# Kernel tuning notes

Hardware: AMD Instinct MI355X
Metric: run time of the kernel (lower is better)

## Reference

```python
import jax, jax.numpy as jnp
import numpy as np

MUL = 16            # multiplicity of 0e and 1o irreps (in and out)
N_NODES = 10000
N_EDGES = 160000
EDGE_FDIM = 128
H_DIM = 128
WNUM = 4 * MUL * MUL  # 4 instructions x (16 u x 1 v x 16 w) = 1024 weights per edge


def setup_inputs() -> dict:
    key = jax.random.key(0)
    ks = jax.random.split(key, 6)
    x = jax.random.normal(ks[0], (N_NODES, 4 * MUL), dtype=jnp.float32)  # 16x0e + 16x1o -> dim 64
    edge_index = jax.random.randint(ks[1], (2, N_EDGES), 0, N_NODES, dtype=jnp.int32)
    edge_attr = jax.random.normal(ks[2], (N_EDGES, EDGE_FDIM), dtype=jnp.float32)
    edge_sh = jax.random.normal(ks[3], (N_EDGES, 4), dtype=jnp.float32)  # 1x0e + 1x1o
    fc_w1 = jax.random.normal(ks[4], (EDGE_FDIM, H_DIM), dtype=jnp.float32) / np.sqrt(EDGE_FDIM)
    fc_b1 = jnp.zeros((H_DIM,), jnp.float32)
    fc_w2 = jax.random.normal(ks[5], (H_DIM, WNUM), dtype=jnp.float32) / np.sqrt(H_DIM)
    fc_b2 = jnp.zeros((WNUM,), jnp.float32)
    return dict(x=x, edge_index=edge_index, edge_attr=edge_attr, edge_sh=edge_sh,
                fc_w1=fc_w1, fc_b1=fc_b1, fc_w2=fc_w2, fc_b2=fc_b2)


def _tensor_product(xe, edge_sh, w):
    """FullyConnectedTensorProduct('16x0e+16x1o', '1x0e+1x1o', '16x0e+16x1o'),
    shared_weights=False. Instructions (uvw, v=1):
      0e x 0e -> 0e ; 0e x 1o -> 1o ; 1o x 0e -> 1o ; 1o x 1o -> 0e (dot / sqrt(3)).
    Path alpha = 1/sqrt(fan_in) with fan_in = 2*MUL per output irrep (2 paths x 16x1)."""
    x0 = xe[:, :MUL]                          # [E, 16] scalars
    x1 = xe[:, MUL:].reshape(-1, MUL, 3)      # [E, 16, 3] vectors
    sh0 = edge_sh[:, 0:1]                     # [E, 1]
    sh1 = edge_sh[:, 1:4]                     # [E, 3]
    wp = w.reshape(-1, 4, MUL, MUL)           # [E, 4 paths, u, w]
    w00, w01, w10, w11 = wp[:, 0], wp[:, 1], wp[:, 2], wp[:, 3]
    alpha = 1.0 / np.sqrt(2.0 * MUL)
    dot = jnp.einsum('eum,em->eu', x1, sh1)   # 1o . 1o -> 0e
    out0 = alpha * (jnp.einsum('eu,euw->ew', x0 * sh0, w00)
                    + jnp.einsum('eu,euw->ew', dot, w11) / np.sqrt(3.0))  # [E, 16]
    out1 = alpha * (jnp.einsum('eu,euw,em->ewm', x0, w01, sh1)
                    + jnp.einsum('eum,euw->ewm', x1 * sh0[:, :, None], w10))  # [E, 16, 3]
    return jnp.concatenate([out0, out1.reshape(-1, 3 * MUL)], axis=-1)  # [E, 64]


def reference(x, edge_index, edge_attr, edge_sh, fc_w1, fc_b1, fc_w2, fc_b2):
    src, dst = edge_index[0], edge_index[1]
    # per-edge tensor-product weights from edge features (dropout p=0 -> identity)
    w = jax.nn.relu(edge_attr @ fc_w1 + fc_b1) @ fc_w2 + fc_b2       # [E, 1024]
    tp_out = _tensor_product(x[src], edge_sh, w)                      # gather + TP
    seg = jax.ops.segment_sum(tp_out, dst, num_segments=N_NODES)      # scatter-add
    cnt = jax.ops.segment_sum(jnp.ones((N_EDGES,), tp_out.dtype), dst, num_segments=N_NODES)
    out = seg / jnp.maximum(cnt, 1.0)[:, None]                        # mean aggregation
    # residual: out_dim == in_dim (64), so F.pad is a no-op
    return out + x
```

## Files before the change

kernel.cpp:

```cpp
#include <hip/hip_runtime.h>
#include <stdint.h>

#define E_TOTAL 160000
#define NODES   10000
#define FDIM    128
#define HDIM    128
#define WN      1024
#define CDIM    64
#define EPB     32
#define NTHR    256

typedef __bf16 bf16x8 __attribute__((ext_vector_type(8)));
typedef __bf16 bf16x4 __attribute__((ext_vector_type(4)));
typedef float  f32x4  __attribute__((ext_vector_type(4)));

#define MFMA16(a,b,c) __builtin_amdgcn_mfma_f32_16x16x32_bf16(a,b,c,0,0,0)

#define WS_W1B (512*1024)
#define WS_CNT (576*1024)

__device__ __forceinline__ f32x4 ntload4(const float* p) {
    return __builtin_nontemporal_load((const f32x4*)p);
}

__global__ void prep_kernel(const float* __restrict__ W1, const float* __restrict__ W2,
                            __bf16* __restrict__ W1B, __bf16* __restrict__ W2B,
                            float* __restrict__ out_acc, int* __restrict__ cnt) {
    const int b   = blockIdx.x;
    const int tid = threadIdx.x;
    if (b < 72) {
        const float* W = (b < 64) ? W2 : W1;
        __bf16* outB   = (b < 64) ? W2B : W1B;
        const int N    = (b < 64) ? WN : HDIM;
        const int tile = (b < 64) ? b : (b - 64);
        const int lane = tid & 63, ks = tid >> 6;
        const int n  = tile * 16 + (lane & 15);
        const int k0 = ks * 32 + (lane >> 4) * 8;
        bf16x8 hi;
        #pragma unroll
        for (int j = 0; j < 8; ++j) hi[j] = (__bf16)W[(size_t)(k0 + j) * N + n];
        *(bf16x8*)(outB + ((size_t)(tile * 4 + ks) * 64 + lane) * 8) = hi;
    } else {
        const int zt = (b - 72) * NTHR + tid;
        const float4 z4 = make_float4(0.f, 0.f, 0.f, 0.f);
        for (int i = zt; i < NODES * CDIM / 4; i += 8 * NTHR) ((float4*)out_acc)[i] = z4;
        for (int i = zt; i < NODES; i += 8 * NTHR) cnt[i] = 0;
    }
}

__global__ __launch_bounds__(NTHR, 4)
void fused_edge_kernel(const float* __restrict__ x,
                       const int*   __restrict__ edge_index,
                       const float* __restrict__ edge_attr,
                       const float* __restrict__ edge_sh,
                       const float* __restrict__ fc_b1,
                       const float* __restrict__ fc_b2,
                       const __bf16* __restrict__ W1B,
                       const __bf16* __restrict__ W2B,
                       float* __restrict__ out_acc,
                       int*   __restrict__ cnt)
{
    __shared__ float s_f[6][16][EPB];
    __shared__ __align__(16) char s_ab[16384];
    __shared__ float s_b2s[WN];
    __shared__ float s_sh1[3][36];
    __shared__ int   s_dst[EPB];

    __bf16* s_attr = (__bf16*)s_ab;
    __bf16* s_h    = (__bf16*)(s_ab + 8192);

    const int tid  = threadIdx.x;
    const int w    = tid >> 6;
    const int th   = w >> 1;
    const int kh   = w & 1;
    const int lane = tid & 63;
    const int quad = lane >> 4;
    const int li   = lane & 15;
    const int e0   = blockIdx.x * EPB;

    if (lane < 32) {
        const int e  = lane;
        const int up = w * 4;
        const int ge = e0 + e;
        const int src = edge_index[ge];
        const f32x4 sh4 = ntload4(edge_sh + (size_t)ge * 4);
        if (tid < EPB) {
            const int d = edge_index[E_TOTAL + ge];
            s_dst[e] = d;
            atomicAdd(&cnt[d], 1);
            s_sh1[0][e] = sh4.y; s_sh1[1][e] = sh4.z; s_sh1[2][e] = sh4.w;
        }
        const float* xp = x + (size_t)src * CDIM;
        const float4 x0v = *(const float4*)(xp + up);
        const float4 xa  = *(const float4*)(xp + 16 + up * 3);
        const float4 xb  = *(const float4*)(xp + 16 + up * 3 + 4);
        const float4 xc  = *(const float4*)(xp + 16 + up * 3 + 8);
        const float x1v[4][3] = {
            {xa.x, xa.y, xa.z}, {xa.w, xb.x, xb.y},
            {xb.z, xb.w, xc.x}, {xc.y, xc.z, xc.w}};
        const float x0a[4] = {x0v.x, x0v.y, x0v.z, x0v.w};
        const float alpha = 0.17677669529663689f;
        const float ai3   = alpha * 0.57735026918962576f;
        const float sh0 = sh4.x;
        #pragma unroll
        for (int j = 0; j < 4; ++j) {
            const int u = up + j;
            const float x0u = x0a[j];
            s_f[0][u][e] = alpha * sh0 * x0u;
            s_f[1][u][e] = alpha * x0u;
            s_f[2][u][e] = alpha * sh0 * x1v[j][0];
            s_f[3][u][e] = alpha * sh0 * x1v[j][1];
            s_f[4][u][e] = alpha * sh0 * x1v[j][2];
            s_f[5][u][e] = ai3 * (x1v[j][0]*sh4.y + x1v[j][1]*sh4.z + x1v[j][2]*sh4.w);
        }
    }
    #pragma unroll
    for (int t4 = 0; t4 < 4; ++t4) {
        const int t = tid + t4 * NTHR;
        const int e = t >> 5, i4 = t & 31;
        const f32x4 v = ntload4(edge_attr + (size_t)(e0 + e) * FDIM + i4 * 4);
        const int f = i4 >> 3, j0 = (i4 & 1) * 4, qc = (i4 >> 1) & 3;
        const int g = e >> 4, lc = e & 15;
        bf16x4 bv = {(__bf16)v[0], (__bf16)v[1], (__bf16)v[2], (__bf16)v[3]};
        *(bf16x4*)(s_attr + (((f * 2 + g) * 64 + qc * 16 + lc) * 8 + j0)) = bv;
    }
    *(f32x4*)&s_b2s[tid * 4] = *(const f32x4*)(fc_b2 + tid * 4);
    __syncthreads();

    {
        const int nt0 = w * 2;
        const float b1a = fc_b1[nt0 * 16 + li];
        const float b1b = fc_b1[(nt0 + 1) * 16 + li];
        bf16x8 A1[2][4];
        #pragma unroll
        for (int g = 0; g < 2; ++g)
            #pragma unroll
            for (int ks = 0; ks < 4; ++ks)
                A1[g][ks] = *(const bf16x8*)(s_attr + ((ks * 2 + g) * 64 + lane) * 8);
        #pragma unroll
        for (int nt2 = 0; nt2 < 2; ++nt2) {
            const int nt = nt0 + nt2;
            const float bias = nt2 ? b1b : b1a;
            bf16x8 Bf[4];
            #pragma unroll
            for (int ks = 0; ks < 4; ++ks)
                Bf[ks] = *(const bf16x8*)(W1B + ((size_t)(nt * 4 + ks) * 64 + lane) * 8);
            f32x4 acc[2];
            #pragma unroll
            for (int g = 0; g < 2; ++g) acc[g] = (f32x4){bias, bias, bias, bias};
            #pragma unroll
            for (int ks = 0; ks < 4; ++ks)
                #pragma unroll
                for (int g = 0; g < 2; ++g) acc[g] = MFMA16(A1[g][ks], Bf[ks], acc[g]);
            const int f  = nt >> 1;
            const int qc = (2 * (nt & 1) + (li >> 3)) & 3;
            const int j  = li & 7;
            #pragma unroll
            for (int g = 0; g < 2; ++g)
                #pragma unroll
                for (int r = 0; r < 4; ++r)
                    s_h[((f * 2 + g) * 64 + qc * 16 + (quad * 4 + r)) * 8 + j] =
                        (__bf16)fmaxf(acc[g][r], 0.f);
        }
    }
    __syncthreads();

    bf16x8 A2[2][2];
    #pragma unroll
    for (int g = 0; g < 2; ++g)
        #pragma unroll
        for (int k2 = 0; k2 < 2; ++k2)
            A2[g][k2] = *(const bf16x8*)(s_h + (((kh * 2 + k2) * 2 + g) * 64 + lane) * 8);

    f32x4 o0[2];
    f32x4 o1[2][3];
    #pragma unroll
    for (int g = 0; g < 2; ++g) {
        o0[g] = (f32x4){0.f, 0.f, 0.f, 0.f};
        #pragma unroll
        for (int m = 0; m < 3; ++m) o1[g][m] = (f32x4){0.f, 0.f, 0.f, 0.f};
    }
    const int tbase = th * 32;
    const __bf16* Wp = W2B + ((size_t)(tbase * 4 + kh * 2) * 64 + lane) * 8;
    bf16x8 P[2][2];
    #pragma unroll
    for (int s = 0; s < 2; ++s)
        #pragma unroll
        for (int k2 = 0; k2 < 2; ++k2)
            P[s][k2] = *(const bf16x8*)(Wp + (s * 4 + k2) * 512);

    #pragma unroll
    for (int half = 0; half < 2; ++half) {
        #pragma unroll
        for (int cc = 0; cc < 16; ++cc) {
            const int c = half * 16 + cc;
            const int u = cc;
            const bf16x8 b0 = P[c & 1][0];
            const bf16x8 b1 = P[c & 1][1];
            if (c + 2 < 32) {
                #pragma unroll
                for (int k2 = 0; k2 < 2; ++k2)
                    P[c & 1][k2] = *(const bf16x8*)(Wp + ((c + 2) * 4 + k2) * 512);
            }
            f32x4 acc[2];
            if (kh == 0) {
                const float b2v = s_b2s[(tbase + c) * 16 + li];
                acc[0] = (f32x4){b2v, b2v, b2v, b2v};
                acc[1] = acc[0];
            } else {
                acc[0] = (f32x4){0.f, 0.f, 0.f, 0.f};
                acc[1] = acc[0];
            }
            #pragma unroll
            for (int g = 0; g < 2; ++g) {
                acc[g] = MFMA16(A2[g][0], b0, acc[g]);
                acc[g] = MFMA16(A2[g][1], b1, acc[g]);
            }
            if (th == 0) {
                if (half == 0) {
                    #pragma unroll
                    for (int g = 0; g < 2; ++g)
                        o0[g] += *(const f32x4*)&s_f[0][u][g * 16 + quad * 4] * acc[g];
                } else {
                    #pragma unroll
                    for (int g = 0; g < 2; ++g)
                        o1[g][0] += *(const f32x4*)&s_f[1][u][g * 16 + quad * 4] * acc[g];
                }
            } else {
                if (half == 0) {
                    #pragma unroll
                    for (int g = 0; g < 2; ++g)
                        #pragma unroll
                        for (int m = 0; m < 3; ++m)
                            o1[g][m] += *(const f32x4*)&s_f[2 + m][u][g * 16 + quad * 4] * acc[g];
                } else {
                    #pragma unroll
                    for (int g = 0; g < 2; ++g)
                        o0[g] += *(const f32x4*)&s_f[5][u][g * 16 + quad * 4] * acc[g];
                }
            }
        }
    }
    if (th == 0) {
        #pragma unroll
        for (int g = 0; g < 2; ++g) {
            const f32x4 t1 = o1[g][0];
            o1[g][2] = t1 * *(const f32x4*)&s_sh1[2][g * 16 + quad * 4];
            o1[g][1] = t1 * *(const f32x4*)&s_sh1[1][g * 16 + quad * 4];
            o1[g][0] = t1 * *(const f32x4*)&s_sh1[0][g * 16 + quad * 4];
        }
    }

    __syncthreads();
    float* regA = (float*)s_ab;
    float* regB = (float*)(s_ab + 8192);
    float* regC = &s_f[0][0][0];
    float* dump = (kh == 1) ? ((th == 0) ? regA : regB) : ((th == 1) ? regC : nullptr);
    if (dump) {
        #pragma unroll
        for (int g = 0; g < 2; ++g)
            #pragma unroll
            for (int r = 0; r < 4; ++r) {
                float* row = dump + (g * 16 + quad * 4 + r) * 64;
                row[li] = o0[g][r];
                #pragma unroll
                for (int m = 0; m < 3; ++m) row[16 + li * 3 + m] = o1[g][m][r];
            }
    }
    __syncthreads();
    if (kh == 0 && th == 0) {
        #pragma unroll
        for (int g = 0; g < 2; ++g)
            #pragma unroll
            for (int r = 0; r < 4; ++r) {
                const int e = g * 16 + quad * 4 + r;
                const float* rA = regA + e * 64;
                const float* rB = regB + e * 64;
                const float* rC = regC + e * 64;
                float* op = out_acc + (size_t)s_dst[e] * CDIM;
                unsafeAtomicAdd(&op[li], o0[g][r] + rA[li] + rB[li] + rC[li]);
                #pragma unroll
                for (int m = 0; m < 3; ++m) {
                    const int s = 16 + li * 3 + m;
                    unsafeAtomicAdd(&op[s], o1[g][m][r] + rA[s] + rB[s] + rC[s]);
                }
            }
    }
}

__global__ void finalize_kernel(const float* __restrict__ x,
                                const int*   __restrict__ cnt,
                                float*       __restrict__ out)
{
    const int idx = blockIdx.x * blockDim.x + threadIdx.x;
    if (idx < NODES * CDIM) {
        const int n = idx >> 6;
        const float c = (float)(cnt[n] > 1 ? cnt[n] : 1);
        out[idx] = out[idx] / c + x[idx];
    }
}

extern "C" void kernel_launch(void* const* d_in, const int* in_sizes, int n_in,
                              void* d_out, int out_size, void* d_ws, size_t ws_size,
                              hipStream_t stream) {
    (void)in_sizes; (void)n_in; (void)out_size; (void)ws_size;
    const float* x          = (const float*)d_in[0];
    const int*   edge_index = (const int*)  d_in[1];
    const float* edge_attr  = (const float*)d_in[2];
    const float* edge_sh    = (const float*)d_in[3];
    const float* fc_w1      = (const float*)d_in[4];
    const float* fc_b1      = (const float*)d_in[5];
    const float* fc_w2      = (const float*)d_in[6];
    const float* fc_b2      = (const float*)d_in[7];
    float*  out = (float*)d_out;
    __bf16* W2B = (__bf16*)d_ws;
    __bf16* W1B = (__bf16*)((char*)d_ws + WS_W1B);
    int*    cnt = (int*)((char*)d_ws + WS_CNT);

    prep_kernel<<<80, NTHR, 0, stream>>>(fc_w1, fc_w2, W1B, W2B, out, cnt);
    fused_edge_kernel<<<E_TOTAL / EPB, NTHR, 0, stream>>>(
        x, edge_index, edge_attr, edge_sh, fc_b1, fc_b2, W1B, W2B, out, cnt);
    finalize_kernel<<<(NODES * CDIM + NTHR - 1) / NTHR, NTHR, 0, stream>>>(x, cnt, out);
}
```

Before: 253.9 us.

## Shrink LDS via arena aliasing, raise occupancy, spread atomic reduction across waves

Shared memory is packed into one aliased arena: s_attr and s_h now share storage, guarded by an extra barrier. This cuts per-block LDS so launch bounds can ask for 6 blocks per SM. The W2 prefetch depth doubles from 2 to 4 stages, and the cross-wave reduction becomes a pairwise padded-LDS sum so all 256 threads issue the atomics instead of one wave doing 32. The prep kernel also gets more zeroing blocks with a grid-derived stride. The higher occupancy target may force register spills, especially with the deeper prefetch buffers.

```diff
diff --git a/kernel.cpp b/kernel.cpp
--- a/kernel.cpp
+++ b/kernel.cpp
@@ -41,14 +41,16 @@
         for (int j = 0; j < 8; ++j) hi[j] = (__bf16)W[(size_t)(k0 + j) * N + n];
         *(bf16x8*)(outB + ((size_t)(tile * 4 + ks) * 64 + lane) * 8) = hi;
     } else {
-        const int zt = (b - 72) * NTHR + tid;
+        const int zt     = (b - 72) * NTHR + tid;
+        const int stride = ((int)gridDim.x - 72) * NTHR;
         const float4 z4 = make_float4(0.f, 0.f, 0.f, 0.f);
-        for (int i = zt; i < NODES * CDIM / 4; i += 8 * NTHR) ((float4*)out_acc)[i] = z4;
-        for (int i = zt; i < NODES; i += 8 * NTHR) cnt[i] = 0;
-    }
-}
-
-__global__ __launch_bounds__(NTHR, 4)
+        for (int i = zt; i < NODES * CDIM / 4; i += stride) ((float4*)out_acc)[i] = z4;
+        for (int i = zt; i < NODES; i += stride) cnt[i] = 0;
+    }
+}
+
+#define ZS 68
+__global__ __launch_bounds__(NTHR, 6)
 void fused_edge_kernel(const float* __restrict__ x,
                        const int*   __restrict__ edge_index,
                        const float* __restrict__ edge_attr,
@@ -60,14 +62,13 @@
                        float* __restrict__ out_acc,
                        int*   __restrict__ cnt)
 {
-    __shared__ float s_f[6][16][EPB];
-    __shared__ __align__(16) char s_ab[16384];
-    __shared__ float s_b2s[WN];
-    __shared__ float s_sh1[3][36];
-    __shared__ int   s_dst[EPB];
-
-    __bf16* s_attr = (__bf16*)s_ab;
-    __bf16* s_h    = (__bf16*)(s_ab + 8192);
+    __shared__ __align__(16) char s_arena[25152];
+    __bf16* s_attr = (__bf16*)s_arena;
+    __bf16* s_h    = (__bf16*)s_arena;
+    float (*s_f)[16][32] = (float (*)[16][32])(s_arena + 8192);
+    float*  s_b2s  = (float*)(s_arena + 20480);
+    float (*s_sh1)[36] = (float (*)[36])(s_arena + 24576);
+    int*    s_dst  = (int*)(s_arena + 25024);
 
     const int tid  = threadIdx.x;
     const int w    = tid >> 6;
@@ -137,6 +138,7 @@
             #pragma unroll
             for (int ks = 0; ks < 4; ++ks)
                 A1[g][ks] = *(const bf16x8*)(s_attr + ((ks * 2 + g) * 64 + lane) * 8);
+        __syncthreads();
         #pragma unroll
         for (int nt2 = 0; nt2 < 2; ++nt2) {
             const int nt = nt0 + nt2;
@@ -182,9 +184,9 @@
     }
     const int tbase = th * 32;
     const __bf16* Wp = W2B + ((size_t)(tbase * 4 + kh * 2) * 64 + lane) * 8;
-    bf16x8 P[2][2];
-    #pragma unroll
-    for (int s = 0; s < 2; ++s)
+    bf16x8 P[4][2];
+    #pragma unroll
+    for (int s = 0; s < 4; ++s)
         #pragma unroll
         for (int k2 = 0; k2 < 2; ++k2)
             P[s][k2] = *(const bf16x8*)(Wp + (s * 4 + k2) * 512);
@@ -195,12 +197,12 @@
         for (int cc = 0; cc < 16; ++cc) {
             const int c = half * 16 + cc;
             const int u = cc;
-            const bf16x8 b0 = P[c & 1][0];
-            const bf16x8 b1 = P[c & 1][1];
-            if (c + 2 < 32) {
+            const bf16x8 b0 = P[c & 3][0];
+            const bf16x8 b1 = P[c & 3][1];
+            if (c + 4 < 32) {
                 #pragma unroll
                 for (int k2 = 0; k2 < 2; ++k2)
-                    P[c & 1][k2] = *(const bf16x8*)(Wp + ((c + 2) * 4 + k2) * 512);
+                    P[c & 3][k2] = *(const bf16x8*)(Wp + ((c + 4) * 4 + k2) * 512);
             }
             f32x4 acc[2];
             if (kh == 0) {
@@ -251,40 +253,50 @@
         }
     }
 
+    float* zA = (float*)s_arena;
+    float* zB = (float*)(s_arena + 8704);
     __syncthreads();
-    float* regA = (float*)s_ab;
-    float* regB = (float*)(s_ab + 8192);
-    float* regC = &s_f[0][0][0];
-    float* dump = (kh == 1) ? ((th == 0) ? regA : regB) : ((th == 1) ? regC : nullptr);
-    if (dump) {
-        #pragma unroll
-        for (int g = 0; g < 2; ++g)
-            #pragma unroll
-            for (int r = 0; r < 4; ++r) {
-                float* row = dump + (g * 16 + quad * 4 + r) * 64;
-                row[li] = o0[g][r];
-                #pragma unroll
-                for (int m = 0; m < 3; ++m) row[16 + li * 3 + m] = o1[g][m][r];
-            }
+    {
+        float* zm = (th == 0) ? zA : zB;
+        if (kh == 1) {
+            #pragma unroll
+            for (int g = 0; g < 2; ++g)
+                #pragma unroll
+                for (int r = 0; r < 4; ++r) {
+                    float* row = zm + (g * 16 + quad * 4 + r) * ZS;
+                    row[li] = o0[g][r];
+                    #pragma unroll
+                    for (int m = 0; m < 3; ++m) row[16 + li * 3 + m] = o1[g][m][r];
+                }
+        }
+        __syncthreads();
+        if (kh == 0) {
+            #pragma unroll
+            for (int g = 0; g < 2; ++g)
+                #pragma unroll
+                for (int r = 0; r < 4; ++r) {
+                    float* row = zm + (g * 16 + quad * 4 + r) * ZS;
+                    row[li] += o0[g][r];
+                    #pragma unroll
+                    for (int m = 0; m < 3; ++m) row[16 + li * 3 + m] += o1[g][m][r];
+                }
+        }
     }
     __syncthreads();
-    if (kh == 0 && th == 0) {
-        #pragma unroll
-        for (int g = 0; g < 2; ++g)
-            #pragma unroll
-            for (int r = 0; r < 4; ++r) {
-                const int e = g * 16 + quad * 4 + r;
-                const float* rA = regA + e * 64;
-                const float* rB = regB + e * 64;
-                const float* rC = regC + e * 64;
-                float* op = out_acc + (size_t)s_dst[e] * CDIM;
-                unsafeAtomicAdd(&op[li], o0[g][r] + rA[li] + rB[li] + rC[li]);
-                #pragma unroll
-                for (int m = 0; m < 3; ++m) {
-                    const int s = 16 + li * 3 + m;
-                    unsafeAtomicAdd(&op[s], o1[g][m][r] + rA[s] + rB[s] + rC[s]);
-                }
-            }
+    {
+        const int e  = w * 8 + (lane >> 3);
+        const int j0 = (lane & 7) * 8;
+        const float* ra = zA + e * ZS + j0;
+        const float* rb = zB + e * ZS + j0;
+        const f32x4 a0 = *(const f32x4*)ra;
+        const f32x4 a1 = *(const f32x4*)(ra + 4);
+        const f32x4 c0 = *(const f32x4*)rb;
+        const f32x4 c1 = *(const f32x4*)(rb + 4);
+        float* op = out_acc + (size_t)s_dst[e] * CDIM + j0;
+        #pragma unroll
+        for (int j = 0; j < 4; ++j) unsafeAtomicAdd(&op[j], a0[j] + c0[j]);
+        #pragma unroll
+        for (int j = 0; j < 4; ++j) unsafeAtomicAdd(&op[4 + j], a1[j] + c1[j]);
     }
 }
 
@@ -317,7 +329,7 @@
     __bf16* W1B = (__bf16*)((char*)d_ws + WS_W1B);
     int*    cnt = (int*)((char*)d_ws + WS_CNT);
 
-    prep_kernel<<<80, NTHR, 0, stream>>>(fc_w1, fc_w2, W1B, W2B, out, cnt);
+    prep_kernel<<<256, NTHR, 0, stream>>>(fc_w1, fc_w2, W1B, W2B, out, cnt);
     fused_edge_kernel<<<E_TOTAL / EPB, NTHR, 0, stream>>>(
         x, edge_index, edge_attr, edge_sh, fc_b1, fc_b2, W1B, W2B, out, cnt);
     finalize_kernel<<<(NODES * CDIM + NTHR - 1) / NTHR, NTHR, 0, stream>>>(x, cnt, out);
```

New measurement: 670.0 us. +163.9%, slower.
